# Kernel optimization log

Hardware: AMD Instinct MI355X
Metric: run time of the kernel (lower is better)

The kernel has to match this reference:

```python
import jax, jax.numpy as jnp
import numpy as np

B, N, F, H, L = 4, 512, 128, 4, 2
HID = 128            # edge MLP hidden width
LAM = 5.0            # sinkhorn_lambda
ITERS = 10           # sinkhorn_iter
NEG_SLOPE = 0.2      # GAT leaky-relu slope


def setup_inputs() -> dict:
    key = jax.random.key(0)
    ks = jax.random.split(key, 10)
    sc = 0.05
    return {
        "joint_features": jax.random.normal(ks[0], (B, N, F), jnp.float32),
        "joint_coords": jax.random.normal(ks[1], (B, N, 3), jnp.float32),
        # edge MLP: Linear(2F+1 -> 128), Linear(128 -> 1)
        "W1": jax.random.normal(ks[2], (2 * F + 1, HID), jnp.float32) * sc,
        "b1": jnp.zeros((HID,), jnp.float32),
        "W2": jax.random.normal(ks[3], (HID, 1), jnp.float32) * sc,
        "b2": jnp.zeros((1,), jnp.float32),
        # GAT layers (stacked over L): W (F -> H*F), attention vecs a_src/a_dst (H,F), bias (F)
        "Wg": jax.random.normal(ks[4], (L, F, H * F), jnp.float32) * sc,
        "a_src": jax.random.normal(ks[5], (L, H, F), jnp.float32) * sc,
        "a_dst": jax.random.normal(ks[6], (L, H, F), jnp.float32) * sc,
        "bg": jnp.zeros((L, F), jnp.float32),
    }


def _forward(joint_features, joint_coords, W1, b1, W2, b2, Wg, a_src, a_dst, bg):
    Bc, Nc, Fc = joint_features.shape
    # pairwise euclidean distances (B,N,N)  == torch.cdist(p=2)
    diff = joint_coords[:, :, None, :] - joint_coords[:, None, :, :]
    dist = jnp.sqrt(jnp.maximum(jnp.sum(diff * diff, axis=-1), 0.0))
    # edge MLP on cat([feat_i, feat_j, dist]). Fuse the concat by splitting W1
    # into row blocks: [W_a (F,HID); W_b (F,HID); w_d (HID,)] -- same math,
    # avoids materializing the (B,N,N,2F+1) concat tensor.
    Wa, Wb, wd = W1[:Fc], W1[Fc:2 * Fc], W1[2 * Fc]
    ha = joint_features @ Wa                      # (B,N,HID)
    hb = joint_features @ Wb                      # (B,N,HID)
    hidden = jax.nn.relu(ha[:, :, None, :] + hb[:, None, :, :]
                         + dist[..., None] * wd + b1)   # (B,N,N,HID)
    cost = jnp.squeeze(hidden @ W2, -1) + b2[0]         # (B,N,N)
    # Sinkhorn normalization: K = exp(-lambda * C), alternate row/col scaling
    def sink_step(P, _):
        P = P / jnp.sum(P, axis=-1, keepdims=True)
        P = P / jnp.sum(P, axis=-2, keepdims=True)
        return P, None
    adj, _ = jax.lax.scan(sink_step, jnp.exp(-LAM * cost), None, length=ITERS)
    # adj is strictly positive -> to_sparse() yields the fully-connected graph
    # per batch; GATConv(heads=H, concat=False) becomes dense attention over N.
    x = joint_features
    nlayers, nheads = Wg.shape[0], a_src.shape[1]
    for l in range(nlayers):
        xw = (x @ Wg[l]).reshape(Bc, Nc, nheads, Fc)            # (B,N,H,F)
        s_src = jnp.einsum('bnhf,hf->bnh', xw, a_src[l])        # sender score
        s_dst = jnp.einsum('bnhf,hf->bnh', xw, a_dst[l])        # receiver score
        # e[b,i,j,h]: message j -> i
        e = jax.nn.leaky_relu(s_dst[:, :, None, :] + s_src[:, None, :, :], NEG_SLOPE)
        attn = jax.nn.softmax(e, axis=2)                        # softmax over senders j
        x = jnp.einsum('bijh,bjhf->bihf', attn, xw).mean(axis=2) + bg[l]
    final_adj = jax.nn.sigmoid(jnp.einsum('bif,bjf->bij', x, x))
    return final_adj, adj


def reference(joint_features, joint_coords, W1, b1, W2, b2, Wg, a_src, a_dst, bg):
    return _forward(joint_features, joint_coords, W1, b1, W2, b2, Wg, a_src, a_dst, bg)
```

## Files before the change

### kernel.cpp

```cpp
#include <hip/hip_runtime.h>
#include <math.h>

#define NB 4
#define NN 512

__global__ void kA(const float* __restrict__ X, const float* __restrict__ W1,
                   const float* __restrict__ b1, float* __restrict__ ha,
                   float* __restrict__ hb, float* __restrict__ ru) {
  int b = blockIdx.y, n0 = blockIdx.x * 8;
  __shared__ float xs[8][128];
  int t = threadIdx.x;
  for (int q = t; q < 1024; q += 128) {
    int r = q >> 7, f = q & 127;
    xs[r][f] = X[(size_t)(b * NN + n0 + r) * 128 + f];
  }
  int flat = b * 64 + blockIdx.x;
  if (flat < 16) ru[flat * 128 + t] = 0.f;
  __syncthreads();
  float accA[8] = {0,0,0,0,0,0,0,0}, accB[8] = {0,0,0,0,0,0,0,0};
  for (int f = 0; f < 128; ++f) {
    float wa = W1[f * 128 + t];
    float wb = W1[(128 + f) * 128 + t];
#pragma unroll
    for (int r = 0; r < 8; ++r) {
      accA[r] = fmaf(xs[r][f], wa, accA[r]);
      accB[r] = fmaf(xs[r][f], wb, accB[r]);
    }
  }
  float b1v = b1[t];
#pragma unroll
  for (int r = 0; r < 8; ++r) {
    ha[(size_t)(b * NN + n0 + r) * 128 + t] = accA[r] + b1v;
    hb[(size_t)(b * NN + n0 + r) * 128 + t] = accB[r];
  }
}

__global__ void kB(const float* __restrict__ ha, const float* __restrict__ hb,
                   const float* __restrict__ coords, const float* __restrict__ W1,
                   const float* __restrict__ W2, const float* __restrict__ b2,
                   float* __restrict__ Km, float* __restrict__ ru) {
  int b = blockIdx.z, i0 = blockIdx.y * 32, j0 = blockIdx.x * 32;
  __shared__ alignas(16) float As[32][132];
  __shared__ alignas(16) float Bs[32][132];
  __shared__ alignas(16) float wd[128];
  __shared__ alignas(16) float w2[128];
  __shared__ float ci[32][3], cj[32][3];
  int t = threadIdx.x;
  for (int q = t; q < 1024; q += 256) {
    int r = q >> 5, c = (q & 31) * 4;
    *(float4*)&As[r][c] = *(const float4*)&ha[(size_t)(b * NN + i0 + r) * 128 + c];
    *(float4*)&Bs[r][c] = *(const float4*)&hb[(size_t)(b * NN + j0 + r) * 128 + c];
  }
  if (t < 128) { wd[t] = W1[256 * 128 + t]; w2[t] = W2[t]; }
  if (t < 96) ((float*)ci)[t] = coords[(size_t)(b * NN + i0) * 3 + t];
  else if (t < 192) ((float*)cj)[t - 96] = coords[(size_t)(b * NN + j0) * 3 + (t - 96)];
  __syncthreads();
  int tx = t & 15, ty = t >> 4;
  int ia = 2 * ty, ib = ia + 1, ja = tx, jb = tx + 16;
  float d00, d01, d10, d11;
  {
    float ax = ci[ia][0], ay = ci[ia][1], az = ci[ia][2];
    float bx = ci[ib][0], by = ci[ib][1], bz = ci[ib][2];
    float cx0 = cj[ja][0], cy0 = cj[ja][1], cz0 = cj[ja][2];
    float cx1 = cj[jb][0], cy1 = cj[jb][1], cz1 = cj[jb][2];
    float dx, dy, dz;
    dx = ax - cx0; dy = ay - cy0; dz = az - cz0;
    d00 = sqrtf(fmaxf(dx * dx + dy * dy + dz * dz, 0.f));
    dx = ax - cx1; dy = ay - cy1; dz = az - cz1;
    d01 = sqrtf(fmaxf(dx * dx + dy * dy + dz * dz, 0.f));
    dx = bx - cx0; dy = by - cy0; dz = bz - cz0;
    d10 = sqrtf(fmaxf(dx * dx + dy * dy + dz * dz, 0.f));
    dx = bx - cx1; dy = by - cy1; dz = bz - cz1;
    d11 = sqrtf(fmaxf(dx * dx + dy * dy + dz * dz, 0.f));
  }
  float a00 = 0, a01 = 0, a10 = 0, a11 = 0;
  for (int k = 0; k < 128; k += 4) {
    float4 A0 = *(float4*)&As[ia][k];
    float4 A1 = *(float4*)&As[ib][k];
    float4 B0 = *(float4*)&Bs[ja][k];
    float4 B1 = *(float4*)&Bs[jb][k];
    float4 W = *(float4*)&wd[k];
    float4 V = *(float4*)&w2[k];
#pragma unroll
    for (int kk = 0; kk < 4; ++kk) {
      float av = ((float*)&A0)[kk], av1 = ((float*)&A1)[kk];
      float bv = ((float*)&B0)[kk], bv1 = ((float*)&B1)[kk];
      float wv = ((float*)&W)[kk], vv = ((float*)&V)[kk];
      float t00 = fmaxf(fmaf(d00, wv, av + bv), 0.f);
      float t01 = fmaxf(fmaf(d01, wv, av + bv1), 0.f);
      float t10 = fmaxf(fmaf(d10, wv, av1 + bv), 0.f);
      float t11 = fmaxf(fmaf(d11, wv, av1 + bv1), 0.f);
      a00 = fmaf(t00, vv, a00);
      a01 = fmaf(t01, vv, a01);
      a10 = fmaf(t10, vv, a10);
      a11 = fmaf(t11, vv, a11);
    }
  }
  float b2v = b2[0];
  float k00 = __expf(-5.0f * (a00 + b2v));
  float k01 = __expf(-5.0f * (a01 + b2v));
  float k10 = __expf(-5.0f * (a10 + b2v));
  float k11 = __expf(-5.0f * (a11 + b2v));
  size_t r0 = (size_t)(b * NN + i0 + ia) * NN + j0;
  size_t r1 = (size_t)(b * NN + i0 + ib) * NN + j0;
  Km[r0 + ja] = k00; Km[r0 + jb] = k01;
  Km[r1 + ja] = k10; Km[r1 + jb] = k11;
  float s0 = k00 + k01, s1 = k10 + k11;
#pragma unroll
  for (int off = 1; off < 16; off <<= 1) {
    s0 += __shfl_xor(s0, off);
    s1 += __shfl_xor(s1, off);
  }
  if (tx == 0) {
    atomicAdd(&ru[b * NN + i0 + ia], s0);
    atomicAdd(&ru[b * NN + i0 + ib], s1);
  }
}


__device__ __forceinline__ void dCcol(const float* __restrict__ Km,
                                      const float* __restrict__ ru,
                                      float* __restrict__ rvp,
                                      float* sm, int ic, int b) {
  float* uinv = sm;
  int t = threadIdx.x;
  if (t < 32) uinv[t] = 1.0f / ru[b * NN + ic * 32 + t];
  __syncthreads();
  const float* Kp = Km + (size_t)(b * NN + ic * 32) * NN + t;
  float acc = 0.f;
#pragma unroll 8
  for (int ii = 0; ii < 32; ++ii) acc = fmaf(Kp[(size_t)ii * NN], uinv[ii], acc);
  rvp[ic * 2048 + b * NN + t] = acc;
}

__device__ __forceinline__ void dCrc(const float* __restrict__ Km,
                                     const float* __restrict__ rvpOld,
                                     float* __restrict__ rvpNew,
                                     float* __restrict__ ru,
                                     float* sm, int ic, int b) {
  float* vinv = sm;
  float* uinv = sm + 512;
  int t = threadIdx.x;
  {
    float s = 0.f;
#pragma unroll
    for (int q = 0; q < 16; ++q) s += rvpOld[q * 2048 + b * NN + t];
    vinv[t] = 1.0f / s;
  }
  __syncthreads();
  int w = t >> 6, l = t & 63;
#pragma unroll
  for (int m = 0; m < 4; ++m) {
    int r = ic * 32 + w * 4 + m;
    const float* Kp = Km + (size_t)(b * NN + r) * NN;
    float acc = 0.f;
#pragma unroll
    for (int mm = 0; mm < 8; ++mm) acc = fmaf(Kp[l + 64 * mm], vinv[l + 64 * mm], acc);
#pragma unroll
    for (int off = 1; off < 64; off <<= 1) acc += __shfl_xor(acc, off);
    if (l == 0) { uinv[w * 4 + m] = 1.0f / acc; ru[b * NN + r] = acc; }
  }
  __syncthreads();
  {
    const float* Kp = Km + (size_t)(b * NN + ic * 32) * NN + t;
    float acc = 0.f;
#pragma unroll 8
    for (int ii = 0; ii < 32; ++ii) acc = fmaf(Kp[(size_t)ii * NN], uinv[ii], acc);
    rvpNew[ic * 2048 + b * NN + t] = acc;
  }
}

__device__ __forceinline__ void dG1f(const float* __restrict__ x,
                                     const float* __restrict__ Wg,
                                     const float* __restrict__ asrc,
                                     const float* __restrict__ adst,
                                     float* __restrict__ xw,
                                     float* __restrict__ ssT,
                                     float* __restrict__ sdT,
                                     float* sm, int bx, int b) {
  int n0 = bx * 8;
  float* xs = sm;
  float* red = sm + 1024;
  int t = threadIdx.x;
  for (int q = t; q < 1024; q += 512)
    xs[q] = x[(size_t)(b * NN + n0 + (q >> 7)) * 128 + (q & 127)];
  __syncthreads();
  int c = t;
  float acc[8] = {0,0,0,0,0,0,0,0};
  for (int f = 0; f < 128; ++f) {
    float w0 = Wg[f * 512 + c];
#pragma unroll
    for (int r = 0; r < 8; ++r) acc[r] = fmaf(xs[r * 128 + f], w0, acc[r]);
  }
#pragma unroll
  for (int r = 0; r < 8; ++r)
    xw[(size_t)(b * NN + n0 + r) * 512 + c] = acc[r];
  float asv = asrc[c], adv = adst[c];
  int w = t >> 6, l = t & 63;
#pragma unroll
  for (int r = 0; r < 8; ++r) {
    float ps = acc[r] * asv, pd = acc[r] * adv;
#pragma unroll
    for (int off = 1; off < 64; off <<= 1) {
      ps += __shfl_xor(ps, off);
      pd += __shfl_xor(pd, off);
    }
    if (l == 0) { red[w * 16 + r * 2] = ps; red[w * 16 + r * 2 + 1] = pd; }
  }
  __syncthreads();
  if (t < 64) {
    int h = t >> 4, rr = t & 7, sd = (t >> 3) & 1;
    float s = red[(2 * h) * 16 + rr * 2 + sd] + red[(2 * h + 1) * 16 + rr * 2 + sd];
    float* dst = sd ? sdT : ssT;
    dst[(size_t)(b * 4 + h) * 512 + n0 + rr] = s;
  }
}

#define PLT 520
__device__ __forceinline__ void dG2t(const float* __restrict__ xw,
                                     const float* __restrict__ ssT,
                                     const float* __restrict__ sdT,
                                     float* __restrict__ partial,
                                     float* sm, int bx, int b) {
  int h = bx & 3, i0 = (bx >> 2) * 8;
  int bh = b * 4 + h;
  float* pls = sm;
  float* ssb = sm + 8192;
  float* sdl = sm + 8704;
  float* smaxsh = sm + 8712;
  float* mxl = sm + 8720;
  int t = threadIdx.x;
  {
    float v = ssT[(size_t)bh * 512 + t];
    ssb[t] = v;
#pragma unroll
    for (int off = 1; off < 64; off <<= 1) v = fmaxf(v, __shfl_xor(v, off));
    if ((t & 63) == 0) smaxsh[t >> 6] = v;
  }
  if (t < 8) sdl[t] = sdT[(size_t)bh * 512 + i0 + t];
  __syncthreads();
  if (t < 8) {
    float m = smaxsh[0];
#pragma unroll
    for (int q = 1; q < 8; ++q) m = fmaxf(m, smaxsh[q]);
    float mm = sdl[t] + m;
    mxl[t] = (mm >= 0.f) ? mm : 0.2f * mm;
  }
  __syncthreads();
  {
    int il = t >> 6, jq = t & 63;
    float mx = mxl[il], sdv = sdl[il];
    float pe[8];
    float den = 0.f;
#pragma unroll
    for (int jj = 0; jj < 8; ++jj) {
      int j = jj * 64 + jq;
      float e = sdv + ssb[j];
      e = (e >= 0.f) ? e : 0.2f * e;
      pe[jj] = __expf(e - mx);
      den += pe[jj];
    }
#pragma unroll
    for (int off = 1; off < 64; off <<= 1) den += __shfl_xor(den, off);
    float inv = 1.0f / (4.0f * den);
#pragma unroll
    for (int jj = 0; jj < 8; ++jj) pls[il * PLT + jj * 64 + jq] = pe[jj] * inv;
  }
  __syncthreads();
  int fq = t & 31, jh = t >> 5;
  const float* xp = xw + (size_t)(b * NN) * 512 + h * 128 + fq * 4;
  float4 acc[8];
#pragma unroll
  for (int r = 0; r < 8; ++r) acc[r] = make_float4(0.f, 0.f, 0.f, 0.f);
  int jbase = jh * 32;
#pragma unroll 4
  for (int jj = 0; jj < 32; ++jj) {
    int j = jbase + jj;
    float4 xv = *(const float4*)&xp[(size_t)j * 512];
#pragma unroll
    for (int r = 0; r < 8; ++r) {
      float p = pls[r * PLT + j];
      acc[r].x = fmaf(p, xv.x, acc[r].x);
      acc[r].y = fmaf(p, xv.y, acc[r].y);
      acc[r].z = fmaf(p, xv.z, acc[r].z);
      acc[r].w = fmaf(p, xv.w, acc[r].w);
    }
  }
  __syncthreads();
  int w = t >> 6;
#pragma unroll
  for (int r = 0; r < 8; ++r) {
    acc[r].x += __shfl_xor(acc[r].x, 32);
    acc[r].y += __shfl_xor(acc[r].y, 32);
    acc[r].z += __shfl_xor(acc[r].z, 32);
    acc[r].w += __shfl_xor(acc[r].w, 32);
  }
  float4* sc4 = (float4*)sm;
  if ((t & 63) < 32) {
#pragma unroll
    for (int r = 0; r < 8; ++r) sc4[w * 256 + r * 32 + fq] = acc[r];
  }
  __syncthreads();
  if (t < 256) {
    int r = t >> 5, ff = t & 31;
    float4 s = make_float4(0.f, 0.f, 0.f, 0.f);
#pragma unroll
    for (int q = 0; q < 8; ++q) {
      float4 u = sc4[q * 256 + r * 32 + ff];
      s.x += u.x; s.y += u.y; s.z += u.z; s.w += u.w;
    }
    *(float4*)&partial[((size_t)bh * NN + i0 + r) * 128 + ff * 4] = s;
  }
}

__device__ __forceinline__ void dRed(const float* __restrict__ partial,
                                     const float* __restrict__ bg,
                                     float* __restrict__ xo, int bx, int b) {
  int idx = bx * 512 + threadIdx.x;
  int f4 = idx & 31, i = idx >> 5;
  const float* pp = partial + (((size_t)b * 4) * NN + i) * 128 + f4 * 4;
  float4 s = *(const float4*)pp;
  const float* p1 = pp + (size_t)NN * 128;
  const float* p2 = pp + (size_t)2 * NN * 128;
  const float* p3 = pp + (size_t)3 * NN * 128;
  float4 v1 = *(const float4*)p1, v2 = *(const float4*)p2, v3 = *(const float4*)p3;
  float4 bb = *(const float4*)&bg[f4 * 4];
  s.x += v1.x + v2.x + v3.x + bb.x;
  s.y += v1.y + v2.y + v3.y + bb.y;
  s.z += v1.z + v2.z + v3.z + bb.z;
  s.w += v1.w + v2.w + v3.w + bb.w;
  *(float4*)&xo[(size_t)(b * NN + i) * 128 + f4 * 4] = s;
}

__device__ __forceinline__ void dF(const float* __restrict__ x,
                                   float* __restrict__ out,
                                   float* sm, int fid, int b) {
  int i0 = (fid >> 4) * 32, j0 = (fid & 15) * 32;
  float* As = sm;
  float* Bs = sm + 4224;
  int t = threadIdx.x;
  for (int q = t; q < 1024; q += 512) {
    int r = q >> 5, c = (q & 31) * 4;
    *(float4*)&As[r * 132 + c] = *(const float4*)&x[(size_t)(b * NN + i0 + r) * 128 + c];
    *(float4*)&Bs[r * 132 + c] = *(const float4*)&x[(size_t)(b * NN + j0 + r) * 128 + c];
  }
  __syncthreads();
  int tx = t & 31, ty = t >> 5;
  int ia = 2 * ty, ib = ia + 1;
  float a0 = 0.f, a1 = 0.f;
  for (int k = 0; k < 128; k += 4) {
    float4 A0 = *(float4*)&As[ia * 132 + k];
    float4 A1 = *(float4*)&As[ib * 132 + k];
    float4 B0 = *(float4*)&Bs[tx * 132 + k];
#pragma unroll
    for (int kk = 0; kk < 4; ++kk) {
      a0 = fmaf(((float*)&A0)[kk], ((float*)&B0)[kk], a0);
      a1 = fmaf(((float*)&A1)[kk], ((float*)&B0)[kk], a1);
    }
  }
  out[(size_t)(b * NN + i0 + ia) * NN + j0 + tx] = 1.0f / (1.0f + __expf(-a0));
  out[(size_t)(b * NN + i0 + ib) * NN + j0 + tx] = 1.0f / (1.0f + __expf(-a1));
}


__global__ __launch_bounds__(512) void nCcolG1f(
    const float* Km, const float* ru, float* rvpA,
    const float* X, const float* Wg, const float* as_, const float* ad_,
    float* xw, float* ssT, float* sdT) {
  __shared__ alignas(16) float sm[1280];
  if (blockIdx.x < 16) dCcol(Km, ru, rvpA, sm, blockIdx.x, blockIdx.y);
  else dG1f(X, Wg, as_, ad_, xw, ssT, sdT, sm, blockIdx.x - 16, blockIdx.y);
}

__global__ __launch_bounds__(512) void nCrcG2t(
    const float* Km, const float* rvpOld, float* rvpNew, float* ru,
    const float* xw, const float* ssT, const float* sdT, float* partial) {
  __shared__ alignas(16) float sm[8728];
  if (blockIdx.x < 16) dCrc(Km, rvpOld, rvpNew, ru, sm, blockIdx.x, blockIdx.y);
  else dG2t(xw, ssT, sdT, partial, sm, blockIdx.x - 16, blockIdx.y);
}

__global__ __launch_bounds__(512) void nCrcRed(
    const float* Km, const float* rvpOld, float* rvpNew, float* ru,
    const float* partial, const float* bg, float* xo) {
  __shared__ alignas(16) float sm[544];
  if (blockIdx.x < 16) dCrc(Km, rvpOld, rvpNew, ru, sm, blockIdx.x, blockIdx.y);
  else dRed(partial, bg, xo, blockIdx.x - 16, blockIdx.y);
}

__global__ __launch_bounds__(512) void nCrcG1f(
    const float* Km, const float* rvpOld, float* rvpNew, float* ru,
    const float* x, const float* Wg, const float* as_, const float* ad_,
    float* xw, float* ssT, float* sdT) {
  __shared__ alignas(16) float sm[1280];
  if (blockIdx.x < 16) dCrc(Km, rvpOld, rvpNew, ru, sm, blockIdx.x, blockIdx.y);
  else dG1f(x, Wg, as_, ad_, xw, ssT, sdT, sm, blockIdx.x - 16, blockIdx.y);
}

__global__ __launch_bounds__(512) void nCrcF(
    const float* Km, const float* rvpOld, float* rvpNew, float* ru,
    const float* x, float* outF) {
  __shared__ alignas(16) float sm[8448];
  if (blockIdx.x < 16) dCrc(Km, rvpOld, rvpNew, ru, sm, blockIdx.x, blockIdx.y);
  else dF(x, outF, sm, blockIdx.x - 16, blockIdx.y);
}

__global__ __launch_bounds__(512) void kCrc(
    const float* Km, const float* rvpOld, float* rvpNew, float* ru) {
  __shared__ alignas(16) float sm[544];
  dCrc(Km, rvpOld, rvpNew, ru, sm, blockIdx.x, blockIdx.y);
}

__global__ __launch_bounds__(512) void kAdj(const float* __restrict__ Km,
                                            const float* __restrict__ ru,
                                            const float* __restrict__ rvp,
                                            float* __restrict__ out) {
  int rc = blockIdx.x, b = blockIdx.y;
  __shared__ float vinv[512];
  __shared__ float uinv[32];
  int t = threadIdx.x;
  {
    float s = 0.f;
#pragma unroll
    for (int ic = 0; ic < 16; ++ic) s += rvp[ic * 2048 + b * NN + t];
    vinv[t] = 1.0f / s;
  }
  if (t < 32) uinv[t] = 1.0f / ru[b * NN + rc * 32 + t];
  __syncthreads();
  float vj = vinv[t];
  const float* Kp = Km + (size_t)(b * NN + rc * 32) * NN + t;
  float* op = out + (size_t)(b * NN + rc * 32) * NN + t;
#pragma unroll 4
  for (int m = 0; m < 32; ++m) {
    op[(size_t)m * NN] = Kp[(size_t)m * NN] * uinv[m] * vj;
  }
}

extern "C" void kernel_launch(void* const* d_in, const int* in_sizes, int n_in,
                              void* d_out, int out_size, void* d_ws, size_t ws_size,
                              hipStream_t stream) {
  (void)in_sizes; (void)n_in; (void)out_size; (void)ws_size;
  const float* X   = (const float*)d_in[0];
  const float* C   = (const float*)d_in[1];
  const float* W1  = (const float*)d_in[2];
  const float* b1  = (const float*)d_in[3];
  const float* W2  = (const float*)d_in[4];
  const float* b2  = (const float*)d_in[5];
  const float* Wg  = (const float*)d_in[6];
  const float* as_ = (const float*)d_in[7];
  const float* ad_ = (const float*)d_in[8];
  const float* bg  = (const float*)d_in[9];
  float* out = (float*)d_out;
  float* ws = (float*)d_ws;

  float* ha    = ws;
  float* hb    = ws + 262144;
  float* Km    = ws + 524288;
  float* ru    = ws + 1572864;
  float* xw    = ws + 1591296;
  float* ssT   = ws + 2639872;
  float* sdT   = ws + 2648064;
  float* x1    = ws + 2656256;
  float* x2    = ws + 2918400;
  float* rvpA  = ws + 3180544;
  float* rvpB  = ws + 3246080;
  float* adj   = out + 1048576;
  float* partial = out;

  kA<<<dim3(64, 4), 128, 0, stream>>>(X, W1, b1, ha, hb, ru);
  kB<<<dim3(16, 16, 4), 256, 0, stream>>>(ha, hb, C, W1, W2, b2, Km, ru);
  nCcolG1f<<<dim3(80, 4), 512, 0, stream>>>(Km, ru, rvpA,
                                            X, Wg, as_, ad_, xw, ssT, sdT);
  nCrcG2t<<<dim3(272, 4), 512, 0, stream>>>(Km, rvpA, rvpB, ru,
                                            xw, ssT, sdT, partial);
  nCrcRed<<<dim3(48, 4), 512, 0, stream>>>(Km, rvpB, rvpA, ru,
                                           partial, bg, x1);
  nCrcG1f<<<dim3(80, 4), 512, 0, stream>>>(Km, rvpA, rvpB, ru,
                                           x1, Wg + 65536, as_ + 512, ad_ + 512,
                                           xw, ssT, sdT);
  nCrcG2t<<<dim3(272, 4), 512, 0, stream>>>(Km, rvpB, rvpA, ru,
                                            xw, ssT, sdT, partial);
  nCrcRed<<<dim3(48, 4), 512, 0, stream>>>(Km, rvpA, rvpB, ru,
                                           partial, bg + 128, x2);
  nCrcF<<<dim3(272, 4), 512, 0, stream>>>(Km, rvpB, rvpA, ru, x2, out);
  kCrc<<<dim3(16, 4), 512, 0, stream>>>(Km, rvpA, rvpB, ru);
  kCrc<<<dim3(16, 4), 512, 0, stream>>>(Km, rvpB, rvpA, ru);
  kCrc<<<dim3(16, 4), 512, 0, stream>>>(Km, rvpA, rvpB, ru);
  kAdj<<<dim3(16, 4), 512, 0, stream>>>(Km, ru, rvpB, adj);
}
```

Measured before the change: 165.0 us.

## Double GAT aggregation rows per block and spread final product across Sinkhorn launches

The GAT aggregation tile now handles 16 destination rows per block instead of 8, which halves its block count and reuses each loaded xw row for twice as many outputs. The cost is more accumulator registers and a second shared-memory reduction pass. The final sigmoid(x x^T) work is split into four 64-block chunks, each co-scheduled with one of the trailing Sinkhorn row/column steps, replacing the standalone kCrc launches. This fills idle CUs during the small Sinkhorn kernels but makes each of those launches longer.

```diff
diff --git a/kernel.cpp b/kernel.cpp
--- a/kernel.cpp
+++ b/kernel.cpp
@@ -217,18 +217,18 @@
 }
 
 #define PLT 520
-__device__ __forceinline__ void dG2t(const float* __restrict__ xw,
-                                     const float* __restrict__ ssT,
-                                     const float* __restrict__ sdT,
-                                     float* __restrict__ partial,
-                                     float* sm, int bx, int b) {
-  int h = bx & 3, i0 = (bx >> 2) * 8;
+__device__ __forceinline__ void dG2t16(const float* __restrict__ xw,
+                                       const float* __restrict__ ssT,
+                                       const float* __restrict__ sdT,
+                                       float* __restrict__ partial,
+                                       float* sm, int bx, int b) {
+  int h = bx & 3, i0 = (bx >> 2) * 16;
   int bh = b * 4 + h;
   float* pls = sm;
-  float* ssb = sm + 8192;
-  float* sdl = sm + 8704;
-  float* smaxsh = sm + 8712;
-  float* mxl = sm + 8720;
+  float* ssb = sm + 8320;
+  float* sdl = sm + 8832;
+  float* smaxsh = sm + 8848;
+  float* mxl = sm + 8856;
   int t = threadIdx.x;
   {
     float v = ssT[(size_t)bh * 512 + t];
@@ -237,9 +237,9 @@
     for (int off = 1; off < 64; off <<= 1) v = fmaxf(v, __shfl_xor(v, off));
     if ((t & 63) == 0) smaxsh[t >> 6] = v;
   }
-  if (t < 8) sdl[t] = sdT[(size_t)bh * 512 + i0 + t];
-  __syncthreads();
-  if (t < 8) {
+  if (t < 16) sdl[t] = sdT[(size_t)bh * 512 + i0 + t];
+  __syncthreads();
+  if (t < 16) {
     float m = smaxsh[0];
 #pragma unroll
     for (int q = 1; q < 8; ++q) m = fmaxf(m, smaxsh[q]);
@@ -248,37 +248,41 @@
   }
   __syncthreads();
   {
-    int il = t >> 6, jq = t & 63;
-    float mx = mxl[il], sdv = sdl[il];
-    float pe[8];
-    float den = 0.f;
-#pragma unroll
-    for (int jj = 0; jj < 8; ++jj) {
-      int j = jj * 64 + jq;
-      float e = sdv + ssb[j];
-      e = (e >= 0.f) ? e : 0.2f * e;
-      pe[jj] = __expf(e - mx);
-      den += pe[jj];
-    }
-#pragma unroll
-    for (int off = 1; off < 64; off <<= 1) den += __shfl_xor(den, off);
-    float inv = 1.0f / (4.0f * den);
-#pragma unroll
-    for (int jj = 0; jj < 8; ++jj) pls[il * PLT + jj * 64 + jq] = pe[jj] * inv;
+    int w = t >> 6, lane = t & 63;
+#pragma unroll
+    for (int rr = 0; rr < 2; ++rr) {
+      int il = w * 2 + rr;
+      float mx = mxl[il], sdv = sdl[il];
+      float pe[8];
+      float den = 0.f;
+#pragma unroll
+      for (int jj = 0; jj < 8; ++jj) {
+        int j = jj * 64 + lane;
+        float e = sdv + ssb[j];
+        e = (e >= 0.f) ? e : 0.2f * e;
+        pe[jj] = __expf(e - mx);
+        den += pe[jj];
+      }
+#pragma unroll
+      for (int off = 1; off < 64; off <<= 1) den += __shfl_xor(den, off);
+      float inv = 1.0f / (4.0f * den);
+#pragma unroll
+      for (int jj = 0; jj < 8; ++jj) pls[il * PLT + jj * 64 + lane] = pe[jj] * inv;
+    }
   }
   __syncthreads();
   int fq = t & 31, jh = t >> 5;
   const float* xp = xw + (size_t)(b * NN) * 512 + h * 128 + fq * 4;
-  float4 acc[8];
-#pragma unroll
-  for (int r = 0; r < 8; ++r) acc[r] = make_float4(0.f, 0.f, 0.f, 0.f);
+  float4 acc[16];
+#pragma unroll
+  for (int r = 0; r < 16; ++r) acc[r] = make_float4(0.f, 0.f, 0.f, 0.f);
   int jbase = jh * 32;
-#pragma unroll 4
+#pragma unroll 2
   for (int jj = 0; jj < 32; ++jj) {
     int j = jbase + jj;
     float4 xv = *(const float4*)&xp[(size_t)j * 512];
 #pragma unroll
-    for (int r = 0; r < 8; ++r) {
+    for (int r = 0; r < 16; ++r) {
       float p = pls[r * PLT + j];
       acc[r].x = fmaf(p, xv.x, acc[r].x);
       acc[r].y = fmaf(p, xv.y, acc[r].y);
@@ -286,15 +290,15 @@
       acc[r].w = fmaf(p, xv.w, acc[r].w);
     }
   }
-  __syncthreads();
   int w = t >> 6;
 #pragma unroll
-  for (int r = 0; r < 8; ++r) {
+  for (int r = 0; r < 16; ++r) {
     acc[r].x += __shfl_xor(acc[r].x, 32);
     acc[r].y += __shfl_xor(acc[r].y, 32);
     acc[r].z += __shfl_xor(acc[r].z, 32);
     acc[r].w += __shfl_xor(acc[r].w, 32);
   }
+  __syncthreads();
   float4* sc4 = (float4*)sm;
   if ((t & 63) < 32) {
 #pragma unroll
@@ -310,6 +314,22 @@
       s.x += u.x; s.y += u.y; s.z += u.z; s.w += u.w;
     }
     *(float4*)&partial[((size_t)bh * NN + i0 + r) * 128 + ff * 4] = s;
+  }
+  __syncthreads();
+  if ((t & 63) < 32) {
+#pragma unroll
+    for (int r = 0; r < 8; ++r) sc4[w * 256 + r * 32 + fq] = acc[r + 8];
+  }
+  __syncthreads();
+  if (t < 256) {
+    int r = t >> 5, ff = t & 31;
+    float4 s = make_float4(0.f, 0.f, 0.f, 0.f);
+#pragma unroll
+    for (int q = 0; q < 8; ++q) {
+      float4 u = sc4[q * 256 + r * 32 + ff];
+      s.x += u.x; s.y += u.y; s.z += u.z; s.w += u.w;
+    }
+    *(float4*)&partial[((size_t)bh * NN + i0 + 8 + r) * 128 + ff * 4] = s;
   }
 }
 
@@ -375,9 +395,9 @@
 __global__ __launch_bounds__(512) void nCrcG2t(
     const float* Km, const float* rvpOld, float* rvpNew, float* ru,
     const float* xw, const float* ssT, const float* sdT, float* partial) {
-  __shared__ alignas(16) float sm[8728];
+  __shared__ alignas(16) float sm[8872];
   if (blockIdx.x < 16) dCrc(Km, rvpOld, rvpNew, ru, sm, blockIdx.x, blockIdx.y);
-  else dG2t(xw, ssT, sdT, partial, sm, blockIdx.x - 16, blockIdx.y);
+  else dG2t16(xw, ssT, sdT, partial, sm, blockIdx.x - 16, blockIdx.y);
 }
 
 __global__ __launch_bounds__(512) void nCrcRed(
@@ -397,18 +417,12 @@
   else dG1f(x, Wg, as_, ad_, xw, ssT, sdT, sm, blockIdx.x - 16, blockIdx.y);
 }
 
-__global__ __launch_bounds__(512) void nCrcF(
+__global__ __launch_bounds__(512) void nCrcFp(
     const float* Km, const float* rvpOld, float* rvpNew, float* ru,
-    const float* x, float* outF) {
+    const float* x, float* outF, int fbase) {
   __shared__ alignas(16) float sm[8448];
   if (blockIdx.x < 16) dCrc(Km, rvpOld, rvpNew, ru, sm, blockIdx.x, blockIdx.y);
-  else dF(x, outF, sm, blockIdx.x - 16, blockIdx.y);
-}
-
-__global__ __launch_bounds__(512) void kCrc(
-    const float* Km, const float* rvpOld, float* rvpNew, float* ru) {
-  __shared__ alignas(16) float sm[544];
-  dCrc(Km, rvpOld, rvpNew, ru, sm, blockIdx.x, blockIdx.y);
+  else dF(x, outF, sm, fbase + (blockIdx.x - 16), blockIdx.y);
 }
 
 __global__ __launch_bounds__(512) void kAdj(const float* __restrict__ Km,
@@ -471,20 +485,20 @@
   kB<<<dim3(16, 16, 4), 256, 0, stream>>>(ha, hb, C, W1, W2, b2, Km, ru);
   nCcolG1f<<<dim3(80, 4), 512, 0, stream>>>(Km, ru, rvpA,
                                             X, Wg, as_, ad_, xw, ssT, sdT);
-  nCrcG2t<<<dim3(272, 4), 512, 0, stream>>>(Km, rvpA, rvpB, ru,
+  nCrcG2t<<<dim3(144, 4), 512, 0, stream>>>(Km, rvpA, rvpB, ru,
                                             xw, ssT, sdT, partial);
   nCrcRed<<<dim3(48, 4), 512, 0, stream>>>(Km, rvpB, rvpA, ru,
                                            partial, bg, x1);
   nCrcG1f<<<dim3(80, 4), 512, 0, stream>>>(Km, rvpA, rvpB, ru,
                                            x1, Wg + 65536, as_ + 512, ad_ + 512,
                                            xw, ssT, sdT);
-  nCrcG2t<<<dim3(272, 4), 512, 0, stream>>>(Km, rvpB, rvpA, ru,
+  nCrcG2t<<<dim3(144, 4), 512, 0, stream>>>(Km, rvpB, rvpA, ru,
                                             xw, ssT, sdT, partial);
   nCrcRed<<<dim3(48, 4), 512, 0, stream>>>(Km, rvpA, rvpB, ru,
                                            partial, bg + 128, x2);
-  nCrcF<<<dim3(272, 4), 512, 0, stream>>>(Km, rvpB, rvpA, ru, x2, out);
-  kCrc<<<dim3(16, 4), 512, 0, stream>>>(Km, rvpA, rvpB, ru);
-  kCrc<<<dim3(16, 4), 512, 0, stream>>>(Km, rvpB, rvpA, ru);
-  kCrc<<<dim3(16, 4), 512, 0, stream>>>(Km, rvpA, rvpB, ru);
+  nCrcFp<<<dim3(80, 4), 512, 0, stream>>>(Km, rvpB, rvpA, ru, x2, out, 0);
+  nCrcFp<<<dim3(80, 4), 512, 0, stream>>>(Km, rvpA, rvpB, ru, x2, out, 64);
+  nCrcFp<<<dim3(80, 4), 512, 0, stream>>>(Km, rvpB, rvpA, ru, x2, out, 128);
+  nCrcFp<<<dim3(80, 4), 512, 0, stream>>>(Km, rvpA, rvpB, ru, x2, out, 192);
   kAdj<<<dim3(16, 4), 512, 0, stream>>>(Km, ru, rvpB, adj);
 }
```

Measured after the change: 168.1 us. Within noise of the previous version (+1.8%).
